# Kernel tuning notes

Hardware: AMD Instinct MI355X
Metric: run time of the kernel (lower is better)

The kernel has to match this reference:

```python
import math
import jax, jax.numpy as jnp
import numpy as np

VMIN, VMAX = 0.0, 1.0
NUM_BINS = 64
SIGMA = 0.5 * (VMAX - VMIN) / NUM_BINS  # matches torch: sigma * (vmax-vmin)/num_bins
EPS = 1e-10


def setup_inputs() -> dict:
    key = jax.random.key(0)
    k1, k2 = jax.random.split(key)
    shape = (2, 1, 96, 96, 96)
    tar = jax.random.uniform(k1, shape, dtype=jnp.float32)
    src = jax.random.uniform(k2, shape, dtype=jnp.float32)
    return {"tar": tar, "src": src}


def _normalise_minmax(x, min_out, max_out):
    # x: (N, P) -- per-sample min-max normalisation to [min_out, max_out]
    xmin = jnp.min(x, axis=1, keepdims=True)
    xmax = jnp.max(x, axis=1, keepdims=True)
    return (x - xmin) / (xmax - xmin + EPS) * (max_out - min_out) + min_out


def _windowed(x, bins):
    # x: (N, P), bins: (B,) -> (N, B, P) Gaussian kernel weights
    d = x[:, None, :] - bins[None, :, None]
    return jnp.exp(-(d * d) / (2.0 * SIGMA * SIGMA)) / math.sqrt(2.0 * math.pi) * SIGMA


def reference(tar, src):
    N = tar.shape[0]
    # use channel 0 only, flatten spatial dims
    t = _normalise_minmax(tar[:, 0].reshape(N, -1), VMIN, VMAX)
    s = _normalise_minmax(src[:, 0].reshape(N, -1), VMIN, VMAX)

    bins = jnp.linspace(VMIN, VMAX, NUM_BINS, dtype=tar.dtype)
    w_tar = _windowed(t, bins)  # (N, B, P)
    w_src = _windowed(s, bins)  # (N, B, P)

    hist_joint = jnp.einsum('nbp,ncp->nbc', w_tar, w_src)  # (N, B, B)
    hist_norm = jnp.sum(hist_joint, axis=(1, 2), keepdims=True)
    p_joint = hist_joint / hist_norm

    p_tar = jnp.sum(p_joint, axis=2)  # (N, B)
    p_src = jnp.sum(p_joint, axis=1)  # (N, B)

    ent_tar = -jnp.sum(p_tar * jnp.log(p_tar + EPS), axis=1)
    ent_src = -jnp.sum(p_src * jnp.log(p_src + EPS), axis=1)
    ent_joint = -jnp.sum(p_joint * jnp.log(p_joint + EPS), axis=(1, 2))

    # normalised=True branch
    return -jnp.mean((ent_tar + ent_src) / ent_joint)
```

## Files before the change

kernel.cpp:

```cpp
#include <hip/hip_runtime.h>
#include <math.h>

#define NBINS 64
#define HIST_ELEMS (NBINS*NBINS)
#define PTS_PER_BLOCK 3456
#define GXN 256
#define CHUNKS 27
#define LSTRIDE 68
#define SQK 1.7256062f
#define SMEM_FLOATS (2*PTS_PER_BLOCK + NBINS*LSTRIDE)

typedef float f4 __attribute__((ext_vector_type(4)));
typedef float f32x4 __attribute__((ext_vector_type(4)));
typedef _Float16 half8 __attribute__((ext_vector_type(8)));
typedef int int4v __attribute__((ext_vector_type(4)));

static __device__ __forceinline__ half8 pack8(const float* w) {
    int4v v;
    v[0] = __builtin_bit_cast(int, __builtin_amdgcn_cvt_pkrtz(w[0], w[1]));
    v[1] = __builtin_bit_cast(int, __builtin_amdgcn_cvt_pkrtz(w[2], w[3]));
    v[2] = __builtin_bit_cast(int, __builtin_amdgcn_cvt_pkrtz(w[4], w[5]));
    v[3] = __builtin_bit_cast(int, __builtin_amdgcn_cvt_pkrtz(w[6], w[7]));
    return __builtin_bit_cast(half8, v);
}

__global__ __launch_bounds__(256) void minmax_kernel(const float* __restrict__ tar,
                                                     const float* __restrict__ src,
                                                     float* __restrict__ pm,
                                                     unsigned* __restrict__ ctr,
                                                     float* __restrict__ hist, int P) {
    const int b = blockIdx.x, n = blockIdx.y, t = blockIdx.z;
    const f4* x = (const f4*)((t == 0 ? tar : src) + (size_t)n * P);
    const int per = (P / 4) / 64;
    float lmin = INFINITY, lmax = -INFINITY;
    for (int i = b * per + threadIdx.x; i < (b + 1) * per; i += 256) {
        f4 v = x[i];
        lmin = fminf(lmin, fminf(fminf(v[0], v[1]), fminf(v[2], v[3])));
        lmax = fmaxf(lmax, fmaxf(fmaxf(v[0], v[1]), fmaxf(v[2], v[3])));
    }
    for (int off = 32; off > 0; off >>= 1) {
        lmin = fminf(lmin, __shfl_down(lmin, off, 64));
        lmax = fmaxf(lmax, __shfl_down(lmax, off, 64));
    }
    __shared__ float smin[4], smax[4];
    const int lane = threadIdx.x & 63, wave = threadIdx.x >> 6;
    if (lane == 0) { smin[wave] = lmin; smax[wave] = lmax; }
    __syncthreads();
    if (threadIdx.x == 0) {
        pm[(n * 2 + t) * 64 + b] =
            fminf(fminf(smin[0], smin[1]), fminf(smin[2], smin[3]));
        pm[256 + (n * 2 + t) * 64 + b] =
            fmaxf(fmaxf(smax[0], smax[1]), fmaxf(smax[2], smax[3]));
    }
    const int flat = b + 64 * n + 128 * t;
    f4* hz = (f4*)hist + flat * 8;
    const f4 z = {0.f, 0.f, 0.f, 0.f};
    if (threadIdx.x < 8) hz[threadIdx.x] = z;
    if (flat == 0 && threadIdx.x == 0) *ctr = 0u;
}

template <int STAGED>
__global__ __launch_bounds__(256) void mfma_hist_kernel(const float* __restrict__ tar,
                                                        const float* __restrict__ src,
                                                        const float* __restrict__ pm,
                                                        float* __restrict__ bh,
                                                        float* __restrict__ hist,
                                                        int P) {
    const int n = blockIdx.y;
    const int bx = blockIdx.x;
    const int tid = threadIdx.x;
    const int lane = tid & 63, wave = tid >> 6;
    const int mlane = lane & 15, quad = lane >> 4;

    __shared__ float smem[SMEM_FLOATS];
    __shared__ float mmred[4];
    float* su_t = smem;
    float* su_s = smem + PTS_PER_BLOCK;
    float* lh = smem + 2 * PTS_PER_BLOCK;

    if (wave == 0) {
        float a = pm[(n * 2 + 0) * 64 + lane];
        float b = pm[256 + (n * 2 + 0) * 64 + lane];
        float c = pm[(n * 2 + 1) * 64 + lane];
        float d = pm[256 + (n * 2 + 1) * 64 + lane];
        for (int off = 32; off > 0; off >>= 1) {
            a = fminf(a, __shfl_down(a, off, 64));
            b = fmaxf(b, __shfl_down(b, off, 64));
            c = fminf(c, __shfl_down(c, off, 64));
            d = fmaxf(d, __shfl_down(d, off, 64));
        }
        if (lane == 0) { mmred[0] = a; mmred[1] = b; mmred[2] = c; mmred[3] = d; }
    }

    {
        const f4* tg = (const f4*)(tar + (size_t)n * P + (size_t)bx * PTS_PER_BLOCK);
        const f4* sg = (const f4*)(src + (size_t)n * P + (size_t)bx * PTS_PER_BLOCK);
        f4* st4 = (f4*)su_t;
        f4* ss4 = (f4*)su_s;
        #pragma unroll
        for (int k = 0; k < 3; ++k) {
            const int i = tid + k * 256;
            st4[i] = tg[i];
            ss4[i] = sg[i];
        }
        if (tid < 96) {
            const int i = 768 + tid;
            st4[i] = tg[i];
            ss4[i] = sg[i];
        }
    }
    __syncthreads();

    const float tmin = mmred[0], tmax = mmred[1];
    const float smin = mmred[2], smax = mmred[3];
    const float tk = 63.0f / (tmax - tmin + 1e-10f) * SQK;
    const float sk = 63.0f / (smax - smin + 1e-10f) * SQK;
    float mt2[4], ms2[4];
    #pragma unroll
    for (int mt = 0; mt < 4; ++mt) {
        const float b = SQK * (float)(mlane + 16 * mt);
        mt2[mt] = tmin * tk + b;
        ms2[mt] = smin * sk + b;
    }

    f32x4 acc[4][4];
    #pragma unroll
    for (int a = 0; a < 4; ++a)
        #pragma unroll
        for (int b = 0; b < 4; ++b) acc[a][b] = (f32x4){0.f, 0.f, 0.f, 0.f};

    const int kwbase = wave * (32 * CHUNKS) + quad * 8;
    #pragma unroll 3
    for (int c = 0; c < CHUNKS; ++c) {
        const int kbase = kwbase + c * 32;
        const f4* pt4 = (const f4*)&su_t[kbase];
        const f4* ps4 = (const f4*)&su_s[kbase];
        f4 ta = pt4[0], tb = pt4[1];
        f4 sa = ps4[0], sb = ps4[1];
        float xt[8] = {ta[0], ta[1], ta[2], ta[3], tb[0], tb[1], tb[2], tb[3]};
        float xs[8] = {sa[0], sa[1], sa[2], sa[3], sb[0], sb[1], sb[2], sb[3]};

        half8 af[4], bf[4];
        #pragma unroll
        for (int mt = 0; mt < 4; ++mt) {
            float w[8];
            #pragma unroll
            for (int j = 0; j < 8; ++j) {
                float d = fmaf(xt[j], tk, -mt2[mt]);
                w[j] = __builtin_amdgcn_exp2f(-(d * d));
            }
            af[mt] = pack8(w);
        }
        #pragma unroll
        for (int nt = 0; nt < 4; ++nt) {
            float w[8];
            #pragma unroll
            for (int j = 0; j < 8; ++j) {
                float d = fmaf(xs[j], sk, -ms2[nt]);
                w[j] = __builtin_amdgcn_exp2f(-(d * d));
            }
            bf[nt] = pack8(w);
        }
        #pragma unroll
        for (int mt = 0; mt < 4; ++mt)
            #pragma unroll
            for (int nt = 0; nt < 4; ++nt)
                acc[mt][nt] = __builtin_amdgcn_mfma_f32_16x16x32_f16(
                    af[mt], bf[nt], acc[mt][nt], 0, 0, 0);
    }

    #pragma unroll
    for (int w = 0; w < 4; ++w) {
        if (wave == w) {
            #pragma unroll
            for (int nt = 0; nt < 4; ++nt)
                #pragma unroll
                for (int mt = 0; mt < 4; ++mt) {
                    f4* p = (f4*)&lh[(16 * nt + mlane) * LSTRIDE + 16 * mt + 4 * quad];
                    if (w == 0) {
                        *p = acc[mt][nt];
                    } else {
                        f4 v = *p;
                        v += acc[mt][nt];
                        *p = v;
                    }
                }
        }
        __syncthreads();
    }

    if (STAGED) {
        f4* dst = (f4*)(bh + ((size_t)n * GXN + bx) * HIST_ELEMS);
        #pragma unroll
        for (int k = 0; k < 4; ++k) {
            const int i4 = tid + k * 256;
            const int c = i4 >> 4, r4 = (i4 & 15) * 4;
            dst[i4] = *(const f4*)&lh[c * LSTRIDE + r4];
        }
    } else {
        float* gh = hist + (size_t)n * HIST_ELEMS;
        for (int i = tid; i < HIST_ELEMS; i += 256) {
            const int c = i >> 6, r = i & 63;
            unsafeAtomicAdd(&gh[i], lh[c * LSTRIDE + r]);
        }
    }
}

__global__ __launch_bounds__(256) void reduce_finalize_kernel(const float* __restrict__ bh,
                                                              float* __restrict__ hist,
                                                              unsigned* __restrict__ ctr,
                                                              float* __restrict__ out,
                                                              int staged) {
    const int tid = threadIdx.x;
    const int lane = tid & 63, wave = tid >> 6;
    __shared__ float h2[2 * HIST_ELEMS];
    __shared__ float buf[4], rowsum[NBINS], colsum[NBINS], colp[4 * NBINS];
    __shared__ int lastflag;

    if (staged) {
        const int g = blockIdx.x * 256 + tid;
        const int n = g >> 12, e = g & 4095;
        const float* p = bh + (((size_t)n * GXN) << 12) + e;
        float sum = 0.0f;
        #pragma unroll 8
        for (int b = 0; b < GXN; ++b) sum += p[(size_t)b << 12];
        hist[g] = sum;
    }

    __threadfence();
    if (tid == 0) {
        unsigned old = atomicAdd(ctr, 1u);
        lastflag = (old == 31) ? 1 : 0;
    }
    __syncthreads();
    if (!lastflag) return;

    for (int i = tid; i < 2 * HIST_ELEMS; i += 256)
        h2[i] = __hip_atomic_load(&hist[i], __ATOMIC_RELAXED, __HIP_MEMORY_SCOPE_SYSTEM);
    __syncthreads();

    float accl = 0.0f;
    for (int nn = 0; nn < 2; ++nn) {
        const float* h = h2 + nn * HIST_ELEMS;
        {
            int r = tid >> 2, q = tid & 3;
            const float* hp = h + r * NBINS + q * 16;
            float sv = 0.0f;
            #pragma unroll
            for (int k = 0; k < 16; ++k) sv += hp[k];
            sv += __shfl_down(sv, 1, 64);
            sv += __shfl_down(sv, 2, 64);
            if (q == 0) rowsum[r] = sv;
        }
        {
            int c = tid & 63, g = tid >> 6;
            const float* hp = h + (g * 16) * NBINS + c;
            float sv = 0.0f;
            #pragma unroll
            for (int k = 0; k < 16; ++k) sv += hp[k * NBINS];
            colp[g * NBINS + c] = sv;
        }
        __syncthreads();
        if (tid < NBINS)
            colsum[tid] = colp[0 * NBINS + tid] + colp[1 * NBINS + tid] +
                          colp[2 * NBINS + tid] + colp[3 * NBINS + tid];
        __syncthreads();

        float tv = (tid < NBINS) ? rowsum[tid] : 0.0f;
        for (int off = 32; off > 0; off >>= 1) tv += __shfl_down(tv, off, 64);
        __syncthreads();
        if (lane == 0) buf[wave] = tv;
        __syncthreads();
        const float total = buf[0] + buf[1] + buf[2] + buf[3];
        const float inv = 1.0f / total;

        float ej = 0.0f;
        for (int i = tid; i < HIST_ELEMS; i += 256) {
            float p = h[i] * inv;
            ej += p * __logf(p + 1e-10f);
        }
        for (int off = 32; off > 0; off >>= 1) ej += __shfl_down(ej, off, 64);
        __syncthreads();
        if (lane == 0) buf[wave] = ej;
        __syncthreads();
        const float entj = -(buf[0] + buf[1] + buf[2] + buf[3]);

        float em = 0.0f;
        if (tid < NBINS) {
            float p = rowsum[tid] * inv;
            em = p * __logf(p + 1e-10f);
        } else if (tid < 2 * NBINS) {
            float p = colsum[tid - NBINS] * inv;
            em = p * __logf(p + 1e-10f);
        }
        for (int off = 32; off > 0; off >>= 1) em += __shfl_down(em, off, 64);
        __syncthreads();
        if (lane == 0) buf[wave] = em;
        __syncthreads();
        const float ents = -(buf[0] + buf[1] + buf[2] + buf[3]);

        accl += ents / entj;
        __syncthreads();
    }
    if (tid == 0) out[0] = -0.5f * accl;
}

extern "C" void kernel_launch(void* const* d_in, const int* in_sizes, int n_in,
                              void* d_out, int out_size, void* d_ws, size_t ws_size,
                              hipStream_t stream) {
    const float* tar = (const float*)d_in[0];
    const float* src = (const float*)d_in[1];
    const int N = 2;
    const int P = in_sizes[0] / N;

    float* pm = (float*)d_ws;
    unsigned* ctr = (unsigned*)((char*)d_ws + 2048);
    float* hist = (float*)((char*)d_ws + 4096);
    float* bh = (float*)((char*)d_ws + 36864);
    float* out = (float*)d_out;

    const size_t need = 36864 + (size_t)2 * GXN * HIST_ELEMS * 4;

    minmax_kernel<<<dim3(64, N, 2), 256, 0, stream>>>(tar, src, pm, ctr, hist, P);
    if (ws_size >= need) {
        mfma_hist_kernel<1><<<dim3(GXN, N), 256, 0, stream>>>(tar, src, pm, bh, hist, P);
        reduce_finalize_kernel<<<32, 256, 0, stream>>>(bh, hist, ctr, out, 1);
    } else {
        mfma_hist_kernel<0><<<dim3(GXN, N), 256, 0, stream>>>(tar, src, pm, bh, hist, P);
        reduce_finalize_kernel<<<32, 256, 0, stream>>>(bh, hist, ctr, out, 0);
    }
}
```

Before: 133.1 us.

## Fuse min-max, histogram and finalize into one persistent kernel with grid barriers

Merges the three launches into one kernel. Each block computes partial min/max while staging its tile, then waits at a spin-wait grid barrier on global counters before normalising. After the per-block histograms are written, a second grid barrier lets all blocks share the cross-block reduction, and the last block to arrive computes the entropies. This removes two kernel launches and the separate min/max pass over the inputs, at the cost of a memset launch and reliance on all 512 blocks being co-resident (launch_bounds 256,3), otherwise the barrier deadlocks.

```diff
diff --git a/kernel.cpp b/kernel.cpp
--- a/kernel.cpp
+++ b/kernel.cpp
@@ -5,6 +5,7 @@
 #define HIST_ELEMS (NBINS*NBINS)
 #define PTS_PER_BLOCK 3456
 #define GXN 256
+#define TOTAL_BLOCKS (2*GXN)
 #define CHUNKS 27
 #define LSTRIDE 68
 #define SQK 1.7256062f
@@ -24,48 +25,21 @@
     return __builtin_bit_cast(half8, v);
 }
 
-__global__ __launch_bounds__(256) void minmax_kernel(const float* __restrict__ tar,
-                                                     const float* __restrict__ src,
-                                                     float* __restrict__ pm,
-                                                     unsigned* __restrict__ ctr,
-                                                     float* __restrict__ hist, int P) {
-    const int b = blockIdx.x, n = blockIdx.y, t = blockIdx.z;
-    const f4* x = (const f4*)((t == 0 ? tar : src) + (size_t)n * P);
-    const int per = (P / 4) / 64;
-    float lmin = INFINITY, lmax = -INFINITY;
-    for (int i = b * per + threadIdx.x; i < (b + 1) * per; i += 256) {
-        f4 v = x[i];
-        lmin = fminf(lmin, fminf(fminf(v[0], v[1]), fminf(v[2], v[3])));
-        lmax = fmaxf(lmax, fmaxf(fmaxf(v[0], v[1]), fmaxf(v[2], v[3])));
-    }
-    for (int off = 32; off > 0; off >>= 1) {
-        lmin = fminf(lmin, __shfl_down(lmin, off, 64));
-        lmax = fmaxf(lmax, __shfl_down(lmax, off, 64));
-    }
-    __shared__ float smin[4], smax[4];
-    const int lane = threadIdx.x & 63, wave = threadIdx.x >> 6;
-    if (lane == 0) { smin[wave] = lmin; smax[wave] = lmax; }
-    __syncthreads();
-    if (threadIdx.x == 0) {
-        pm[(n * 2 + t) * 64 + b] =
-            fminf(fminf(smin[0], smin[1]), fminf(smin[2], smin[3]));
-        pm[256 + (n * 2 + t) * 64 + b] =
-            fmaxf(fmaxf(smax[0], smax[1]), fmaxf(smax[2], smax[3]));
-    }
-    const int flat = b + 64 * n + 128 * t;
-    f4* hz = (f4*)hist + flat * 8;
-    const f4 z = {0.f, 0.f, 0.f, 0.f};
-    if (threadIdx.x < 8) hz[threadIdx.x] = z;
-    if (flat == 0 && threadIdx.x == 0) *ctr = 0u;
+static __device__ __forceinline__ float agent_ld(const float* p) {
+    return __hip_atomic_load(p, __ATOMIC_RELAXED, __HIP_MEMORY_SCOPE_AGENT);
+}
+static __device__ __forceinline__ float sys_ld(const float* p) {
+    return __hip_atomic_load(p, __ATOMIC_RELAXED, __HIP_MEMORY_SCOPE_SYSTEM);
 }
 
 template <int STAGED>
-__global__ __launch_bounds__(256) void mfma_hist_kernel(const float* __restrict__ tar,
-                                                        const float* __restrict__ src,
-                                                        const float* __restrict__ pm,
-                                                        float* __restrict__ bh,
-                                                        float* __restrict__ hist,
-                                                        int P) {
+__global__ __launch_bounds__(256, 3) void mi_fused(const float* __restrict__ tar,
+                                                   const float* __restrict__ src,
+                                                   float* __restrict__ pm,
+                                                   unsigned* __restrict__ ctr,
+                                                   float* __restrict__ bh,
+                                                   float* __restrict__ hist,
+                                                   float* __restrict__ out, int P) {
     const int n = blockIdx.y;
     const int bx = blockIdx.x;
     const int tid = threadIdx.x;
@@ -73,25 +47,16 @@
     const int mlane = lane & 15, quad = lane >> 4;
 
     __shared__ float smem[SMEM_FLOATS];
-    __shared__ float mmred[4];
+    __shared__ float mmred[4], wred[4][4];
+    __shared__ float buf[4], rowsum[NBINS], colsum[NBINS], colp[4 * NBINS];
+    __shared__ float psum[16 * 17];
+    __shared__ int lastflag;
     float* su_t = smem;
     float* su_s = smem + PTS_PER_BLOCK;
     float* lh = smem + 2 * PTS_PER_BLOCK;
 
-    if (wave == 0) {
-        float a = pm[(n * 2 + 0) * 64 + lane];
-        float b = pm[256 + (n * 2 + 0) * 64 + lane];
-        float c = pm[(n * 2 + 1) * 64 + lane];
-        float d = pm[256 + (n * 2 + 1) * 64 + lane];
-        for (int off = 32; off > 0; off >>= 1) {
-            a = fminf(a, __shfl_down(a, off, 64));
-            b = fmaxf(b, __shfl_down(b, off, 64));
-            c = fminf(c, __shfl_down(c, off, 64));
-            d = fmaxf(d, __shfl_down(d, off, 64));
-        }
-        if (lane == 0) { mmred[0] = a; mmred[1] = b; mmred[2] = c; mmred[3] = d; }
-    }
-
+    float lmin_t = INFINITY, lmax_t = -INFINITY;
+    float lmin_s = INFINITY, lmax_s = -INFINITY;
     {
         const f4* tg = (const f4*)(tar + (size_t)n * P + (size_t)bx * PTS_PER_BLOCK);
         const f4* sg = (const f4*)(src + (size_t)n * P + (size_t)bx * PTS_PER_BLOCK);
@@ -100,14 +65,60 @@
         #pragma unroll
         for (int k = 0; k < 3; ++k) {
             const int i = tid + k * 256;
-            st4[i] = tg[i];
-            ss4[i] = sg[i];
+            f4 tv = tg[i], sv = sg[i];
+            st4[i] = tv; ss4[i] = sv;
+            lmin_t = fminf(lmin_t, fminf(fminf(tv[0], tv[1]), fminf(tv[2], tv[3])));
+            lmax_t = fmaxf(lmax_t, fmaxf(fmaxf(tv[0], tv[1]), fmaxf(tv[2], tv[3])));
+            lmin_s = fminf(lmin_s, fminf(fminf(sv[0], sv[1]), fminf(sv[2], sv[3])));
+            lmax_s = fmaxf(lmax_s, fmaxf(fmaxf(sv[0], sv[1]), fmaxf(sv[2], sv[3])));
         }
         if (tid < 96) {
             const int i = 768 + tid;
-            st4[i] = tg[i];
-            ss4[i] = sg[i];
-        }
+            f4 tv = tg[i], sv = sg[i];
+            st4[i] = tv; ss4[i] = sv;
+            lmin_t = fminf(lmin_t, fminf(fminf(tv[0], tv[1]), fminf(tv[2], tv[3])));
+            lmax_t = fmaxf(lmax_t, fmaxf(fmaxf(tv[0], tv[1]), fmaxf(tv[2], tv[3])));
+            lmin_s = fminf(lmin_s, fminf(fminf(sv[0], sv[1]), fminf(sv[2], sv[3])));
+            lmax_s = fmaxf(lmax_s, fmaxf(fmaxf(sv[0], sv[1]), fmaxf(sv[2], sv[3])));
+        }
+    }
+    for (int off = 32; off > 0; off >>= 1) {
+        lmin_t = fminf(lmin_t, __shfl_down(lmin_t, off, 64));
+        lmax_t = fmaxf(lmax_t, __shfl_down(lmax_t, off, 64));
+        lmin_s = fminf(lmin_s, __shfl_down(lmin_s, off, 64));
+        lmax_s = fmaxf(lmax_s, __shfl_down(lmax_s, off, 64));
+    }
+    if (lane == 0) {
+        wred[0][wave] = lmin_t; wred[1][wave] = lmax_t;
+        wred[2][wave] = lmin_s; wred[3][wave] = lmax_s;
+    }
+    __syncthreads();
+    if (tid == 0) {
+        pm[0 * 512 + n * 256 + bx] = fminf(fminf(wred[0][0], wred[0][1]), fminf(wred[0][2], wred[0][3]));
+        pm[1 * 512 + n * 256 + bx] = fmaxf(fmaxf(wred[1][0], wred[1][1]), fmaxf(wred[1][2], wred[1][3]));
+        pm[2 * 512 + n * 256 + bx] = fminf(fminf(wred[2][0], wred[2][1]), fminf(wred[2][2], wred[2][3]));
+        pm[3 * 512 + n * 256 + bx] = fmaxf(fmaxf(wred[3][0], wred[3][1]), fmaxf(wred[3][2], wred[3][3]));
+        __threadfence();
+        atomicAdd(&ctr[0], 1u);
+        while (__hip_atomic_load(&ctr[0], __ATOMIC_RELAXED, __HIP_MEMORY_SCOPE_AGENT)
+               < (unsigned)TOTAL_BLOCKS)
+            __builtin_amdgcn_s_sleep(2);
+    }
+    __syncthreads();
+    __threadfence();
+
+    {
+        const float* a = pm + wave * 512 + n * 256;
+        float v0 = agent_ld(a + lane),       v1 = agent_ld(a + lane + 64);
+        float v2 = agent_ld(a + lane + 128), v3 = agent_ld(a + lane + 192);
+        const bool ismax = (wave == 1) || (wave == 3);
+        float v = ismax ? fmaxf(fmaxf(v0, v1), fmaxf(v2, v3))
+                        : fminf(fminf(v0, v1), fminf(v2, v3));
+        for (int off = 32; off > 0; off >>= 1) {
+            float o = __shfl_down(v, off, 64);
+            v = ismax ? fmaxf(v, o) : fminf(v, o);
+        }
+        if (lane == 0) mmred[wave] = v;
     }
     __syncthreads();
 
@@ -197,6 +208,33 @@
             const int c = i4 >> 4, r4 = (i4 & 15) * 4;
             dst[i4] = *(const f4*)&lh[c * LSTRIDE + r4];
         }
+        if (tid == 0) {
+            __threadfence();
+            atomicAdd(&ctr[1], 1u);
+            while (__hip_atomic_load(&ctr[1], __ATOMIC_RELAXED, __HIP_MEMORY_SCOPE_AGENT)
+                   < (unsigned)TOTAL_BLOCKS)
+                __builtin_amdgcn_s_sleep(2);
+        }
+        __syncthreads();
+        __threadfence();
+        {
+            const int flat = n * GXN + bx;
+            const int g0 = flat * 16;
+            const int nn = g0 >> 12, ee0 = g0 & 4095;
+            const int eo = tid & 15, tc = tid >> 4;
+            float s = 0.0f;
+            #pragma unroll
+            for (int k = 0; k < 16; ++k)
+                s += sys_ld(&bh[(((size_t)nn * GXN + tc * 16 + k) << 12) + ee0 + eo]);
+            psum[eo * 17 + tc] = s;
+            __syncthreads();
+            if (tid < 16) {
+                float t = 0.0f;
+                #pragma unroll
+                for (int c = 0; c < 16; ++c) t += psum[tid * 17 + c];
+                hist[g0 + tid] = t;
+            }
+        }
     } else {
         float* gh = hist + (size_t)n * HIST_ELEMS;
         for (int i = tid; i < HIST_ELEMS; i += 256) {
@@ -204,39 +242,18 @@
             unsafeAtomicAdd(&gh[i], lh[c * LSTRIDE + r]);
         }
     }
-}
-
-__global__ __launch_bounds__(256) void reduce_finalize_kernel(const float* __restrict__ bh,
-                                                              float* __restrict__ hist,
-                                                              unsigned* __restrict__ ctr,
-                                                              float* __restrict__ out,
-                                                              int staged) {
-    const int tid = threadIdx.x;
-    const int lane = tid & 63, wave = tid >> 6;
-    __shared__ float h2[2 * HIST_ELEMS];
-    __shared__ float buf[4], rowsum[NBINS], colsum[NBINS], colp[4 * NBINS];
-    __shared__ int lastflag;
-
-    if (staged) {
-        const int g = blockIdx.x * 256 + tid;
-        const int n = g >> 12, e = g & 4095;
-        const float* p = bh + (((size_t)n * GXN) << 12) + e;
-        float sum = 0.0f;
-        #pragma unroll 8
-        for (int b = 0; b < GXN; ++b) sum += p[(size_t)b << 12];
-        hist[g] = sum;
-    }
 
     __threadfence();
     if (tid == 0) {
-        unsigned old = atomicAdd(ctr, 1u);
-        lastflag = (old == 31) ? 1 : 0;
+        unsigned old = atomicAdd(&ctr[2], 1u);
+        lastflag = (old == TOTAL_BLOCKS - 1) ? 1 : 0;
     }
     __syncthreads();
     if (!lastflag) return;
-
-    for (int i = tid; i < 2 * HIST_ELEMS; i += 256)
-        h2[i] = __hip_atomic_load(&hist[i], __ATOMIC_RELAXED, __HIP_MEMORY_SCOPE_SYSTEM);
+    __threadfence();
+
+    float* h2 = smem;
+    for (int i = tid; i < 2 * HIST_ELEMS; i += 256) h2[i] = sys_ld(&hist[i]);
     __syncthreads();
 
     float accl = 0.0f;
@@ -313,20 +330,18 @@
     const int N = 2;
     const int P = in_sizes[0] / N;
 
-    float* pm = (float*)d_ws;
-    unsigned* ctr = (unsigned*)((char*)d_ws + 2048);
-    float* hist = (float*)((char*)d_ws + 4096);
-    float* bh = (float*)((char*)d_ws + 36864);
+    unsigned* ctr = (unsigned*)d_ws;
+    float* pm = (float*)((char*)d_ws + 1024);
+    float* hist = (float*)((char*)d_ws + 16384);
+    float* bh = (float*)((char*)d_ws + 65536);
     float* out = (float*)d_out;
 
-    const size_t need = 36864 + (size_t)2 * GXN * HIST_ELEMS * 4;
-
-    minmax_kernel<<<dim3(64, N, 2), 256, 0, stream>>>(tar, src, pm, ctr, hist, P);
+    const size_t need = 65536 + (size_t)2 * GXN * HIST_ELEMS * 4;
+
+    hipMemsetAsync(d_ws, 0, 49152, stream);
     if (ws_size >= need) {
-        mfma_hist_kernel<1><<<dim3(GXN, N), 256, 0, stream>>>(tar, src, pm, bh, hist, P);
-        reduce_finalize_kernel<<<32, 256, 0, stream>>>(bh, hist, ctr, out, 1);
+        mi_fused<1><<<dim3(GXN, N), 256, 0, stream>>>(tar, src, pm, ctr, bh, hist, out, P);
     } else {
-        mfma_hist_kernel<0><<<dim3(GXN, N), 256, 0, stream>>>(tar, src, pm, bh, hist, P);
-        reduce_finalize_kernel<<<32, 256, 0, stream>>>(bh, hist, ctr, out, 0);
-    }
-}
+        mi_fused<0><<<dim3(GXN, N), 256, 0, stream>>>(tar, src, pm, ctr, bh, hist, out, P);
+    }
+}
```

After: 260.0 us. 95.3% more time.
